# Optimization experiments

Hardware: AMD Instinct MI355X
Metric: run time of the kernel (lower is better)

The kernel has to match this reference:

```python
import jax, jax.numpy as jnp
import numpy as np

B, J = 131072, 24
# SMPL skeleton parent indices (root = joint 0)
SMPL_PARENTS = np.array([-1, 0, 0, 0, 1, 2, 3, 4, 5, 6, 7, 8, 9, 9, 9, 12, 13, 14, 16, 17, 18, 19, 20, 21], dtype=np.int64)


def setup_inputs() -> dict:
    key = jax.random.key(0)
    k1, k2 = jax.random.split(key)
    positions = jax.random.normal(k1, (B, J, 3), dtype=jnp.float32)
    rotations = jax.random.normal(k2, (B, J, 4), dtype=jnp.float32)
    return {"parents": SMPL_PARENTS, "positions": positions, "rotations": rotations}


def _quat_to_rotmat(q):
    # q: [B, J, 4] (w, x, y, z); normalize then standard unit-quaternion rotation matrix
    q = q / jnp.linalg.norm(q, axis=-1, keepdims=True)
    qw, qx, qy, qz = q[..., 0], q[..., 1], q[..., 2], q[..., 3]
    x2, y2, z2 = qx + qx, qy + qy, qz + qz
    xx, yy, zz = qx * x2, qy * y2, qz * z2
    xy, yz, xz = qx * y2, qy * z2, qx * z2
    wx, wy, wz = qw * x2, qw * y2, qw * z2
    row0 = jnp.stack([1.0 - (yy + zz), xy - wz, xz + wy], axis=-1)
    row1 = jnp.stack([xy + wz, 1.0 - (xx + zz), yz - wx], axis=-1)
    row2 = jnp.stack([xz - wy, yz + wx, 1.0 - (xx + yy)], axis=-1)
    return jnp.stack([row0, row1, row2], axis=-2)  # [B, J, 3, 3]


def _local_transforms(positions, rotations):
    R = _quat_to_rotmat(rotations)                       # [B, J, 3, 3]
    top = jnp.concatenate([R, positions[..., None]], axis=-1)  # [B, J, 3, 4]
    bottom = jnp.broadcast_to(
        jnp.array([0.0, 0.0, 0.0, 1.0], dtype=rotations.dtype), top.shape[:2] + (1, 4))
    return jnp.concatenate([top, bottom], axis=-2)       # [B, J, 4, 4]


def reference(parents, positions, rotations):
    parents = np.asarray(parents)  # static skeleton topology
    locals_ = _local_transforms(positions, rotations)    # [B, J, 4, 4]
    n_joints = parents.shape[0]
    # Sequential parent-child chain over the (small, static) joint tree.
    g = [locals_[:, 0]]
    for jt in range(1, n_joints):
        g.append(jnp.matmul(g[int(parents[jt])], locals_[:, jt]))
    globals_ = jnp.stack(g, axis=1)                      # [B, J, 4, 4]
    p = globals_[:, :, :, 3]                             # homogeneous positions [B, J, 4]
    return p[:, :, :3] / p[:, :, 3:4]                    # [B, J, 3]
```

## Files before the change

### kernel.cpp

```cpp
#include <hip/hip_runtime.h>


typedef float f32x4 __attribute__((ext_vector_type(4)));

struct M { float r0,r1,r2,r3,r4,r5,r6,r7,r8,tx,ty,tz; };

__device__ __forceinline__ M loc(float a, float b, float c, float d,
                                 float px, float py, float pz) {
    float inv = rsqrtf(a*a + b*b + c*c + d*d);
    float qw = a*inv, qx = b*inv, qy = c*inv, qz = d*inv;
    float x2 = qx+qx, y2 = qy+qy, z2 = qz+qz;
    float xx = qx*x2, yy = qy*y2, zz = qz*z2;
    float xy = qx*y2, yz = qy*z2, xz = qx*z2;
    float wx = qw*x2, wy = qw*y2, wz = qw*z2;
    M m;
    m.r0 = 1.f-(yy+zz); m.r1 = xy-wz;       m.r2 = xz+wy;
    m.r3 = xy+wz;       m.r4 = 1.f-(xx+zz); m.r5 = yz-wx;
    m.r6 = xz-wy;       m.r7 = yz+wx;       m.r8 = 1.f-(xx+yy);
    m.tx = px; m.ty = py; m.tz = pz;
    return m;
}

__device__ __forceinline__ M mul(const M& a, const M& b) {
    M c;
    c.r0 = a.r0*b.r0 + a.r1*b.r3 + a.r2*b.r6;
    c.r1 = a.r0*b.r1 + a.r1*b.r4 + a.r2*b.r7;
    c.r2 = a.r0*b.r2 + a.r1*b.r5 + a.r2*b.r8;
    c.r3 = a.r3*b.r0 + a.r4*b.r3 + a.r5*b.r6;
    c.r4 = a.r3*b.r1 + a.r4*b.r4 + a.r5*b.r7;
    c.r5 = a.r3*b.r2 + a.r4*b.r5 + a.r5*b.r8;
    c.r6 = a.r6*b.r0 + a.r7*b.r3 + a.r8*b.r6;
    c.r7 = a.r6*b.r1 + a.r7*b.r4 + a.r8*b.r7;
    c.r8 = a.r6*b.r2 + a.r7*b.r5 + a.r8*b.r8;
    c.tx = a.r0*b.tx + a.r1*b.ty + a.r2*b.tz + a.tx;
    c.ty = a.r3*b.tx + a.r4*b.ty + a.r5*b.tz + a.ty;
    c.tz = a.r6*b.tx + a.r7*b.ty + a.r8*b.tz + a.tz;
    return c;
}

#define SPB    48
#define NTHR   256
#define GRID   768
#define RPITCH 100
#define PPITCH 73
#define OPITCH 73

constexpr int MT0[6]  = {0,1,2,4,7,10};
constexpr int PR0[6]  = {-1,0,0,1,3,4};
constexpr int MT1[8]  = {0,2,5,8,11,3,6,9};
constexpr int PR1[8]  = {-1,0,1,2,3,0,5,6};
constexpr int MT2[11] = {0,3,6,9,12,15,13,16,18,20,22};
constexpr int PR2[11] = {-1,0,1,2,3,4,3,6,7,8,9};
constexpr int MT3[9]  = {0,3,6,9,14,17,19,21,23};
constexpr int PR3[9]  = {-1,0,1,2,3,4,5,6,7};

template<int NM>
__device__ __forceinline__ void run_chain(const int (&MT)[NM], const int (&PR)[NM],
                                          int WS,
                                          const float* __restrict__ R,
                                          const float* __restrict__ P,
                                          float* __restrict__ O) {
    M G[NM];
    {
        f32x4 q = *(const f32x4*)(R);
        G[0] = loc(q.x, q.y, q.z, q.w, P[0], P[1], P[2]);
    }
    if (WS == 0) { O[0]=G[0].tx; O[1]=G[0].ty; O[2]=G[0].tz; }
#pragma unroll
    for (int k = 1; k < NM; ++k) {
        const int j = MT[k];
        f32x4 q = *(const f32x4*)(R + 4*j);
        M L = loc(q.x, q.y, q.z, q.w, P[3*j], P[3*j+1], P[3*j+2]);
        G[k] = mul(G[PR[k]], L);
        if (k >= WS) { O[3*j]=G[k].tx; O[3*j+1]=G[k].ty; O[3*j+2]=G[k].tz; }
    }
}

__global__ __launch_bounds__(NTHR, 3) void fk_kernel(
    const float* __restrict__ rot,
    const float* __restrict__ pos,
    float*       __restrict__ out,
    int B)
{
    __shared__ __align__(16) float ldsR[SPB * RPITCH];
    __shared__ float ldsP[SPB * PPITCH];
    __shared__ float ldsO[SPB * OPITCH];

    const int t = threadIdx.x;
    const int nch = (B + SPB - 1) / SPB;
    const size_t limR = (size_t)B * 96;
    const size_t limP = (size_t)B * 72;

    const int w = t >> 6, l = t & 63;

    f32x4 vr[5], vp[4];

    int c = blockIdx.x;
    {
        const size_t baseR = (size_t)c * (SPB*96);
        const size_t baseP = (size_t)c * (SPB*72);
#pragma unroll
        for (int i = 0; i < 5; ++i) {
            const bool g = (i < 4) || (t < 128);
            const size_t gi = baseR + (size_t)(i*1024 + 4*t);
            f32x4 v = {0.f,0.f,0.f,0.f};
            if (g && gi < limR) v = *(const f32x4*)(rot + gi);
            vr[i] = v;
        }
#pragma unroll
        for (int i = 0; i < 4; ++i) {
            const bool g = (i < 3) || (t < 96);
            const size_t gi = baseP + (size_t)(i*1024 + 4*t);
            f32x4 v = {0.f,0.f,0.f,0.f};
            if (g && gi < limP) v = *(const f32x4*)(pos + gi);
            vp[i] = v;
        }
    }

    for (; c < nch; c += GRID) {
        __syncthreads();

#pragma unroll
        for (int i = 0; i < 5; ++i) {
            if ((i < 4) || (t < 128)) {
                const int f = i*1024 + 4*t;
                const int s = f / 96, r = f - 96*s;
                float* d = ldsR + s*RPITCH + r;
                d[0]=vr[i].x; d[1]=vr[i].y; d[2]=vr[i].z; d[3]=vr[i].w;
            }
        }
#pragma unroll
        for (int i = 0; i < 4; ++i) {
            if ((i < 3) || (t < 96)) {
                const int f = i*1024 + 4*t;
                const int s = f / 72, r = f - 72*s;
                float* d = ldsP + s*PPITCH + r;
                d[0]=vp[i].x; d[1]=vp[i].y; d[2]=vp[i].z; d[3]=vp[i].w;
            }
        }
        __syncthreads();

        const int cn = c + GRID;
        if (cn < nch) {
            const size_t baseR = (size_t)cn * (SPB*96);
            const size_t baseP = (size_t)cn * (SPB*72);
#pragma unroll
            for (int i = 0; i < 5; ++i) {
                const bool g = (i < 4) || (t < 128);
                const size_t gi = baseR + (size_t)(i*1024 + 4*t);
                f32x4 v = {0.f,0.f,0.f,0.f};
                if (g && gi < limR) v = *(const f32x4*)(rot + gi);
                vr[i] = v;
            }
#pragma unroll
            for (int i = 0; i < 4; ++i) {
                const bool g = (i < 3) || (t < 96);
                const size_t gi = baseP + (size_t)(i*1024 + 4*t);
                f32x4 v = {0.f,0.f,0.f,0.f};
                if (g && gi < limP) v = *(const f32x4*)(pos + gi);
                vp[i] = v;
            }
        }

        const int b = c * SPB + l;
        if ((l < SPB) && (b < B)) {
            const float* R = ldsR + l * RPITCH;
            const float* P = ldsP + l * PPITCH;
            float*       O = ldsO + l * OPITCH;
            switch (w) {
                case 0:  run_chain(MT0, PR0, 0, R, P, O); break;
                case 1:  run_chain(MT1, PR1, 2, R, P, O); break;
                case 2:  run_chain(MT2, PR2, 4, R, P, O); break;
                default: run_chain(MT3, PR3, 4, R, P, O); break;
            }
        }
        __syncthreads();

        const size_t baseP = (size_t)c * (SPB*72);
#pragma unroll
        for (int n = 0; n < 4; ++n) {
            if ((n < 3) || (t < 96)) {
                const int F = n*1024 + 4*t;
                const int s = F / 72, r = F - 72*s;
                const size_t gi = baseP + (size_t)F;
                if (gi < limP) {
                    f32x4 v = { ldsO[s*OPITCH+r+0], ldsO[s*OPITCH+r+1],
                                ldsO[s*OPITCH+r+2], ldsO[s*OPITCH+r+3] };
                    *(f32x4*)(out + gi) = v;
                }
            }
        }
    }
}

extern "C" void kernel_launch(void* const* d_in, const int* in_sizes, int n_in,
                              void* d_out, int out_size, void* d_ws, size_t ws_size,
                              hipStream_t stream) {
    const int B = out_size / 72;
    const void* rot = nullptr;
    const void* pos = nullptr;
    for (int i = 0; i < n_in; ++i) {
        if      (in_sizes[i] == B * 96) rot = d_in[i];
        else if (in_sizes[i] == B * 72) pos = d_in[i];
    }
    if (!rot) rot = d_in[2];
    if (!pos) pos = d_in[1];

    const int nch  = (B + SPB - 1) / SPB;
    const int grid = (nch < GRID) ? nch : GRID;
    fk_kernel<<<grid, NTHR, 0, stream>>>(
        (const float*)rot, (const float*)pos, (float*)d_out, B);
}
```

Measured before the change: 142.2 us.

## Warp-specialize block into producer/consumer waves with double-buffered LDS

Splits each 512-thread block into four compute waves running the joint chains and four memory waves that load the next chunk and store the previous chunk's output. LDS buffers are double-buffered, so global traffic overlaps compute with one barrier per iteration. Samples per chunk go from 48 to 64 so all 64 lanes of each compute wave are used, the grid shrinks to 256 persistent blocks, and output stores become nontemporal. Risks include lower occupancy from the larger LDS footprint and 2 blocks per CU, and idle memory waves during compute.

Measured after the change: 124.0 us. 12.8% less time.

```diff
diff --git a/kernel.cpp b/kernel.cpp
--- a/kernel.cpp
+++ b/kernel.cpp
@@ -38,12 +38,11 @@
     return c;
 }
 
-#define SPB    48
-#define NTHR   256
-#define GRID   768
+#define SPB    64
+#define NTHR   512
+#define GRIDP  256
 #define RPITCH 100
 #define PPITCH 73
-#define OPITCH 73
 
 constexpr int MT0[6]  = {0,1,2,4,7,10};
 constexpr int PR0[6]  = {-1,0,0,1,3,4};
@@ -76,121 +75,127 @@
     }
 }
 
-__global__ __launch_bounds__(NTHR, 3) void fk_kernel(
+__device__ __forceinline__ void load_regs(int c, int mt,
+                                          const float* __restrict__ rot,
+                                          const float* __restrict__ pos,
+                                          size_t limR, size_t limP,
+                                          f32x4 (&vr)[6], f32x4 (&vp)[5]) {
+    const size_t baseR = (size_t)c * (SPB*96);
+    const size_t baseP = (size_t)c * (SPB*72);
+#pragma unroll
+    for (int i = 0; i < 6; ++i) {
+        const size_t gi = baseR + (size_t)(i*1024 + 4*mt);
+        f32x4 v = {0.f,0.f,0.f,0.f};
+        if (gi < limR) v = *(const f32x4*)(rot + gi);
+        vr[i] = v;
+    }
+#pragma unroll
+    for (int i = 0; i < 5; ++i) {
+        const bool g = (i < 4) || (mt < 128);
+        const size_t gi = baseP + (size_t)(i*1024 + 4*mt);
+        f32x4 v = {0.f,0.f,0.f,0.f};
+        if (g && gi < limP) v = *(const f32x4*)(pos + gi);
+        vp[i] = v;
+    }
+}
+
+__device__ __forceinline__ void scatter_lds(int mt,
+                                            float* __restrict__ Rb,
+                                            float* __restrict__ Pb,
+                                            const f32x4 (&vr)[6],
+                                            const f32x4 (&vp)[5]) {
+#pragma unroll
+    for (int i = 0; i < 6; ++i) {
+        const int f = i*1024 + 4*mt;
+        const int s = f / 96, r = f - 96*s;
+        *(f32x4*)(Rb + s*RPITCH + r) = vr[i];
+    }
+#pragma unroll
+    for (int i = 0; i < 5; ++i) {
+        if ((i < 4) || (mt < 128)) {
+            const int f = i*1024 + 4*mt;
+            const int s = f / 72, r = f - 72*s;
+            float* d = Pb + s*PPITCH + r;
+            d[0]=vp[i].x; d[1]=vp[i].y; d[2]=vp[i].z; d[3]=vp[i].w;
+        }
+    }
+}
+
+__device__ __forceinline__ void store_chunk(const float* __restrict__ Ob,
+                                            int c, int mt, size_t limP,
+                                            float* __restrict__ out) {
+    const size_t baseO = (size_t)c * (SPB*72);
+#pragma unroll
+    for (int n = 0; n < 5; ++n) {
+        if ((n < 4) || (mt < 128)) {
+            const int F = n*1024 + 4*mt;
+            const int s = F / 72, r = F - 72*s;
+            const size_t gi = baseO + (size_t)F;
+            if (gi < limP) {
+                f32x4 v = { Ob[s*PPITCH+r+0], Ob[s*PPITCH+r+1],
+                            Ob[s*PPITCH+r+2], Ob[s*PPITCH+r+3] };
+                __builtin_nontemporal_store(v, (f32x4*)(out + gi));
+            }
+        }
+    }
+}
+
+__global__ __launch_bounds__(NTHR, 2) void fk_kernel(
     const float* __restrict__ rot,
     const float* __restrict__ pos,
     float*       __restrict__ out,
     int B)
 {
-    __shared__ __align__(16) float ldsR[SPB * RPITCH];
-    __shared__ float ldsP[SPB * PPITCH];
-    __shared__ float ldsO[SPB * OPITCH];
-
-    const int t = threadIdx.x;
+    __shared__ __align__(16) float ldsR[2][SPB * RPITCH];
+    __shared__ float ldsP[2][SPB * PPITCH];
+    __shared__ float ldsO[2][SPB * PPITCH];
+
+    const int t   = threadIdx.x;
+    const int w   = t >> 6;
+    const bool cw = (w < 4);
+    const int mt  = t & 255;
     const int nch = (B + SPB - 1) / SPB;
     const size_t limR = (size_t)B * 96;
     const size_t limP = (size_t)B * 72;
 
-    const int w = t >> 6, l = t & 63;
-
-    f32x4 vr[5], vp[4];
-
-    int c = blockIdx.x;
-    {
-        const size_t baseR = (size_t)c * (SPB*96);
-        const size_t baseP = (size_t)c * (SPB*72);
-#pragma unroll
-        for (int i = 0; i < 5; ++i) {
-            const bool g = (i < 4) || (t < 128);
-            const size_t gi = baseR + (size_t)(i*1024 + 4*t);
-            f32x4 v = {0.f,0.f,0.f,0.f};
-            if (g && gi < limR) v = *(const f32x4*)(rot + gi);
-            vr[i] = v;
-        }
-#pragma unroll
-        for (int i = 0; i < 4; ++i) {
-            const bool g = (i < 3) || (t < 96);
-            const size_t gi = baseP + (size_t)(i*1024 + 4*t);
-            f32x4 v = {0.f,0.f,0.f,0.f};
-            if (g && gi < limP) v = *(const f32x4*)(pos + gi);
-            vp[i] = v;
-        }
-    }
-
-    for (; c < nch; c += GRID) {
-        __syncthreads();
-
-#pragma unroll
-        for (int i = 0; i < 5; ++i) {
-            if ((i < 4) || (t < 128)) {
-                const int f = i*1024 + 4*t;
-                const int s = f / 96, r = f - 96*s;
-                float* d = ldsR + s*RPITCH + r;
-                d[0]=vr[i].x; d[1]=vr[i].y; d[2]=vr[i].z; d[3]=vr[i].w;
+    const int c0 = blockIdx.x;
+    if (!cw && c0 < nch) {
+        f32x4 vr[6], vp[5];
+        load_regs(c0, mt, rot, pos, limR, limP, vr, vp);
+        scatter_lds(mt, ldsR[0], ldsP[0], vr, vp);
+    }
+    __syncthreads();
+
+    int i = 0, c = c0;
+    for (; c < nch; c += GRIDP, ++i) {
+        const int q = i & 1;
+        if (cw) {
+            const int l = t & 63;
+            const int b = c * SPB + l;
+            if (b < B) {
+                const float* R = &ldsR[q][l * RPITCH];
+                const float* P = &ldsP[q][l * PPITCH];
+                float*       O = &ldsO[q][l * PPITCH];
+                switch (w) {
+                    case 0:  run_chain(MT0, PR0, 0, R, P, O); break;
+                    case 1:  run_chain(MT1, PR1, 2, R, P, O); break;
+                    case 2:  run_chain(MT2, PR2, 4, R, P, O); break;
+                    default: run_chain(MT3, PR3, 4, R, P, O); break;
+                }
             }
-        }
-#pragma unroll
-        for (int i = 0; i < 4; ++i) {
-            if ((i < 3) || (t < 96)) {
-                const int f = i*1024 + 4*t;
-                const int s = f / 72, r = f - 72*s;
-                float* d = ldsP + s*PPITCH + r;
-                d[0]=vp[i].x; d[1]=vp[i].y; d[2]=vp[i].z; d[3]=vp[i].w;
-            }
+        } else {
+            const int cn = c + GRIDP;
+            const bool ldv = (cn < nch);
+            f32x4 vr[6], vp[5];
+            if (ldv) load_regs(cn, mt, rot, pos, limR, limP, vr, vp);
+            if (i > 0) store_chunk(ldsO[q^1], c - GRIDP, mt, limP, out);
+            if (ldv) scatter_lds(mt, ldsR[q^1], ldsP[q^1], vr, vp);
         }
         __syncthreads();
-
-        const int cn = c + GRID;
-        if (cn < nch) {
-            const size_t baseR = (size_t)cn * (SPB*96);
-            const size_t baseP = (size_t)cn * (SPB*72);
-#pragma unroll
-            for (int i = 0; i < 5; ++i) {
-                const bool g = (i < 4) || (t < 128);
-                const size_t gi = baseR + (size_t)(i*1024 + 4*t);
-                f32x4 v = {0.f,0.f,0.f,0.f};
-                if (g && gi < limR) v = *(const f32x4*)(rot + gi);
-                vr[i] = v;
-            }
-#pragma unroll
-            for (int i = 0; i < 4; ++i) {
-                const bool g = (i < 3) || (t < 96);
-                const size_t gi = baseP + (size_t)(i*1024 + 4*t);
-                f32x4 v = {0.f,0.f,0.f,0.f};
-                if (g && gi < limP) v = *(const f32x4*)(pos + gi);
-                vp[i] = v;
-            }
-        }
-
-        const int b = c * SPB + l;
-        if ((l < SPB) && (b < B)) {
-            const float* R = ldsR + l * RPITCH;
-            const float* P = ldsP + l * PPITCH;
-            float*       O = ldsO + l * OPITCH;
-            switch (w) {
-                case 0:  run_chain(MT0, PR0, 0, R, P, O); break;
-                case 1:  run_chain(MT1, PR1, 2, R, P, O); break;
-                case 2:  run_chain(MT2, PR2, 4, R, P, O); break;
-                default: run_chain(MT3, PR3, 4, R, P, O); break;
-            }
-        }
-        __syncthreads();
-
-        const size_t baseP = (size_t)c * (SPB*72);
-#pragma unroll
-        for (int n = 0; n < 4; ++n) {
-            if ((n < 3) || (t < 96)) {
-                const int F = n*1024 + 4*t;
-                const int s = F / 72, r = F - 72*s;
-                const size_t gi = baseP + (size_t)F;
-                if (gi < limP) {
-                    f32x4 v = { ldsO[s*OPITCH+r+0], ldsO[s*OPITCH+r+1],
-                                ldsO[s*OPITCH+r+2], ldsO[s*OPITCH+r+3] };
-                    *(f32x4*)(out + gi) = v;
-                }
-            }
-        }
-    }
+    }
+
+    if (!cw && i > 0)
+        store_chunk(ldsO[(i-1) & 1], c - GRIDP, mt, limP, out);
 }
 
 extern "C" void kernel_launch(void* const* d_in, const int* in_sizes, int n_in,
@@ -207,7 +212,7 @@
     if (!pos) pos = d_in[1];
 
     const int nch  = (B + SPB - 1) / SPB;
-    const int grid = (nch < GRID) ? nch : GRID;
+    const int grid = (nch < GRIDP) ? nch : GRIDP;
     fk_kernel<<<grid, NTHR, 0, stream>>>(
         (const float*)rot, (const float*)pos, (float*)d_out, B);
 }
```
